# Performance work log

Measured on AMD Instinct MI355X. Metric: run time of the kernel, lower is better.

Reference implementation:

```python
import jax, jax.numpy as jnp
import numpy as np
import math

M = 0.2
S = 30.0
COS_M = math.cos(M); SIN_M = math.sin(M)
TH = math.cos(math.pi - M)          # threshold used in torch.where
MM = math.sin(math.pi - M) * M      # linear penalty past threshold
EPS_LS = 0.1                        # CrossEntropyLoss label_smoothing


def _normalize(a, axis=-1):
    return a / jnp.clip(jnp.linalg.norm(a, axis=axis, keepdims=True), 1e-12)


def setup_inputs() -> dict:
    key = jax.random.key(0)
    k1, k2, k3, k4, k5 = jax.random.split(key, 5)
    B, D, C = 2048, 512, 10000
    x = jax.random.normal(k1, (B, D), dtype=jnp.float32)
    label = jax.random.randint(k2, (B,), 0, 1000)  # valid class ids, ~2 per class
    std = math.sqrt(2.0 / (C + D))  # xavier_normal gain=1
    weight = jax.random.normal(k3, (C, D), dtype=jnp.float32) * std    # self.weight (w)
    weight_m = jax.random.normal(k4, (C, D), dtype=jnp.float32) * std  # self.weight_m (wq)
    weight_n = jax.random.uniform(k5, (C, D), dtype=jnp.float32)       # self.weight_n (wk)
    return {"x": x, "label": label, "weight": weight, "weight_m": weight_m, "weight_n": weight_n}


def reference(x, label, weight, weight_m, weight_n):
    B = x.shape[0]
    C = weight.shape[0]
    xn = _normalize(x)                                   # [B, D]

    # ---- AAM (ArcFace) branch ----
    cosine = xn @ _normalize(weight).T                   # [B, C]
    sine = jnp.sqrt(jnp.clip(1.0 - cosine * cosine, 0.0, 1.0))
    phi = cosine * COS_M - sine * SIN_M
    phi = jnp.where(cosine - TH > 0, phi, cosine - MM)
    one_hot = jax.nn.one_hot(label, C, dtype=cosine.dtype)
    output = (one_hot * phi + (1.0 - one_hot) * cosine) * S
    logp = jax.nn.log_softmax(output, axis=-1)
    q_target = one_hot * (1.0 - EPS_LS) + EPS_LS / C     # label smoothing
    aam_loss = -jnp.mean(jnp.sum(q_target * logp, axis=-1))

    # ---- Control-Contrastive branch ----
    label_matrix = label[:, None] == label[None, :]      # [B, B] bool
    q = xn @ _normalize(weight_m[label]).T               # [B, B]
    k = xn @ _normalize(weight_n[label]).T               # [B, B]
    sim = q * k                                          # elementwise, [B, B]

    lm = label_matrix.astype(sim.dtype)
    ap_m = jnp.sum(sim * lm, axis=1) / jnp.sum(lm, axis=1)  # masked row means, [B]
    ap = jnp.diagonal(sim)                                   # [B]
    an = jnp.where(label_matrix, 0.0, sim)                   # [B, B]

    cos_ap = jnp.clip(ap, 0.0, 1.0)
    sin_ap = jnp.sqrt(jnp.clip(1.0 - cos_ap, 0.0, 1.0))
    cos_apm = jnp.clip(ap_m, 0.0, 1.0)
    sin_apm = jnp.sqrt(jnp.clip(1.0 - cos_apm, 0.0, 1.0))
    cos_an = jnp.clip(an, 0.0, 1.0)
    sin_an = jnp.sqrt(jnp.clip(1.0 - cos_an, 0.0, 1.0))

    phi_pm_c = cos_ap * cos_apm - sin_ap * sin_apm       # [B]
    phi_pm_s = jnp.sqrt(jnp.clip(1.0 - phi_pm_c, 0.0, 1.0))
    phi_pm = phi_pm_c * COS_M - phi_pm_s * SIN_M
    logit_neg = 1.0 - phi_pm                              # [B]

    # torch broadcasting [B,B]*[B] -> broadcast over rows (axis 0)
    phi_nm_s = sin_an * cos_apm[None, :] + cos_an * sin_apm[None, :]
    phi_nm_c = jnp.sqrt(jnp.clip(1.0 - phi_nm_s, 0.0, 1.0))
    phi_nm = phi_nm_s * COS_M - phi_nm_c * SIN_M          # [B, B]

    # ragged boolean-indexed logsumexp == masked logsumexp over whole matrix
    lse_n = jax.nn.logsumexp(jnp.where(label_matrix, -jnp.inf, phi_nm))
    lse_neg = jax.nn.logsumexp(logit_neg)
    cc_loss = jax.nn.softplus(lse_n + lse_neg)

    return aam_loss + cc_loss
```

## Files before the change

kernel.cpp:

```cpp
#include <hip/hip_runtime.h>
#include <hip/hip_bf16.h>

typedef unsigned short u16;
typedef unsigned char u8;
typedef unsigned int u32;
typedef _Float16 f16;
typedef _Float16 f16x8 __attribute__((ext_vector_type(8)));
typedef float f32x4 __attribute__((ext_vector_type(4)));
typedef unsigned int u32x4 __attribute__((ext_vector_type(4)));
typedef unsigned int u32x2 __attribute__((ext_vector_type(2)));
typedef long v2i64 __attribute__((ext_vector_type(2)));

constexpr int BATCH = 2048;
constexpr int DIM   = 512;
constexpr int NCLS  = 10000;
constexpr int NPAD  = 10240;

#define F_S     30.0f
#define F_COS_M 0.9800665778412416f
#define F_SIN_M 0.19866933079506122f
#define F_TH   (-0.9800665778412416f)
#define F_MM    0.03973386615901224f

#define G_AAM  1280
#define G_CC    512

static __device__ __forceinline__ float clampf(float v, float lo, float hi) {
    return fminf(fmaxf(v, lo), hi);
}
static __device__ __forceinline__ u32 pk4_fp8(float a, float b, float c, float d) {
    u32 w = __builtin_amdgcn_cvt_pk_fp8_f32(a, b, 0, false);
    w = __builtin_amdgcn_cvt_pk_fp8_f32(c, d, w, true);
    return w;
}
static __device__ __forceinline__ void glds16(const void* g, void* l) {
    __builtin_amdgcn_global_load_lds(
        (const __attribute__((address_space(1))) unsigned int*)g,
        (__attribute__((address_space(3))) unsigned int*)l, 16, 0, 0);
}
static __device__ __forceinline__ float blk_sum(float v, float* sh, int t) {
#pragma unroll
    for (int o = 32; o > 0; o >>= 1) v += __shfl_down(v, o, 64);
    __syncthreads();
    if ((t & 63) == 0) sh[t >> 6] = v;
    __syncthreads();
    return sh[0] + sh[1] + sh[2] + sh[3];
}

__global__ __launch_bounds__(256) void norm_all_kernel(const float* __restrict__ x,
                                                       const float* __restrict__ w,
                                                       const float* __restrict__ wm,
                                                       const float* __restrict__ wn,
                                                       const int* __restrict__ label,
                                                       u8* __restrict__ xnb,
                                                       u8* __restrict__ wb,
                                                       u8* __restrict__ wqb,
                                                       u8* __restrict__ wkb,
                                                       float* __restrict__ zacc) {
    const int t = threadIdx.x, lane = t & 63, wv = t >> 6;
    const int b = blockIdx.x;
    if (b < 33) zacc[b * 256 + t] = 0.f;

    const int row = b * 4 + wv;
    const float* src;
    u8* dst;
    if (row < BATCH) {
        src = x + (size_t)row * DIM;
        dst = xnb + (size_t)row * DIM;
    } else if (row < BATCH + NPAD) {
        const int r = row - BATCH;
        dst = wb + (size_t)r * DIM;
        if (r >= NCLS) {
            u32x2 z = {0, 0};
            *(u32x2*)(dst + lane * 8) = z;
            return;
        }
        src = w + (size_t)r * DIM;
    } else if (row < BATCH + NPAD + BATCH) {
        const int i = row - (BATCH + NPAD);
        src = wm + (size_t)label[i] * DIM;
        dst = wqb + (size_t)i * DIM;
    } else {
        const int i = row - (BATCH + NPAD + BATCH);
        src = wn + (size_t)label[i] * DIM;
        dst = wkb + (size_t)i * DIM;
    }
    const float4 v0 = ((const float4*)src)[lane * 2];
    const float4 v1 = ((const float4*)src)[lane * 2 + 1];
    float s = v0.x * v0.x + v0.y * v0.y + v0.z * v0.z + v0.w * v0.w
            + v1.x * v1.x + v1.y * v1.y + v1.z * v1.z + v1.w * v1.w;
#pragma unroll
    for (int o = 32; o > 0; o >>= 1) s += __shfl_xor(s, o, 64);
    const float inv = 1.0f / fmaxf(sqrtf(s), 1e-12f);
    u32 lo = pk4_fp8(v0.x * inv, v0.y * inv, v0.z * inv, v0.w * inv);
    u32 hi = pk4_fp8(v1.x * inv, v1.y * inv, v1.z * inv, v1.w * inv);
    const int p = 8 * (lane >> 3) + 4 * (lane & 1) + ((lane >> 1) & 3);
    u32x2 o2;
    o2[0] = __shfl(lo, p, 64);
    o2[1] = __shfl(hi, p, 64);
    *(u32x2*)(dst + lane * 8) = o2;
}

__global__ __launch_bounds__(256) void gemm_fused_kernel(const u8* __restrict__ A,
                                                         const u8* __restrict__ Bw,
                                                         const u8* __restrict__ Bq,
                                                         const u8* __restrict__ Bk,
                                                         const int* __restrict__ label,
                                                         float* __restrict__ sumexp,
                                                         float* __restrict__ sumlogit,
                                                         float* __restrict__ philab,
                                                         f16* __restrict__ sim,
                                                         float* __restrict__ msum,
                                                         float* __restrict__ mcnt,
                                                         float* __restrict__ ap) {
    __shared__ __align__(16) u8 sA[128 * 128];
    __shared__ __align__(16) u8 sB[128 * 128];
    __shared__ float red0[128];
    __shared__ float red1[128];

    const int t = threadIdx.x;
    const int lane = t & 63, wave = t >> 6;
    const int fr = lane & 15, quad = lane >> 4;
    const int swz = fr & 7;

    if (t < 128) { red0[t] = 0.f; red1[t] = 0.f; }

    const int srow = t >> 3;
    const int sgs  = (t & 7) ^ (srow & 7);

    if (blockIdx.x < G_AAM) {
        const int flat = blockIdx.x;
        const int xcd = flat & 7, r = flat >> 3;
        const int bm = r & 15;
        const int bn = (r >> 4) * 8 + xcd;

        const int wm = (wave >> 1) * 64, wn = (wave & 1) * 64;
        const u8* ag = A  + (size_t)(bm * 128 + srow) * DIM + sgs * 16;
        const u8* bg = Bw + (size_t)(bn * 128 + srow) * DIM + sgs * 16;

        f32x4 acc[4][4] = {};

        for (int kb = 0; kb < 4; kb++) {
            const int ko = kb * 128;
#pragma unroll
            for (int s = 0; s < 4; s++) {
                glds16(ag + (size_t)(s * 32) * DIM + ko, &sA[s * 4096 + t * 16]);
                glds16(bg + (size_t)(s * 32) * DIM + ko, &sB[s * 4096 + t * 16]);
            }
            __syncthreads();
#pragma unroll
            for (int blkr = 0; blkr < 2; blkr++) {
                const int slot = ((blkr << 2) | quad) ^ swz;
                v2i64 a8[4], b8[4];
#pragma unroll
                for (int f = 0; f < 4; f++) {
                    a8[f] = __builtin_bit_cast(v2i64, *(const u32x4*)&sA[(wm + f * 16 + fr) * 128 + slot * 16]);
                    b8[f] = __builtin_bit_cast(v2i64, *(const u32x4*)&sB[(wn + f * 16 + fr) * 128 + slot * 16]);
                }
#pragma unroll
                for (int i = 0; i < 4; i++)
#pragma unroll
                    for (int j = 0; j < 4; j++) {
                        acc[i][j] = __builtin_amdgcn_mfma_f32_16x16x32_fp8_fp8(a8[i][0], b8[j][0], acc[i][j], 0, 0, 0);
                        acc[i][j] = __builtin_amdgcn_mfma_f32_16x16x32_fp8_fp8(a8[i][1], b8[j][1], acc[i][j], 0, 0, 0);
                    }
            }
            __syncthreads();
        }

#pragma unroll
        for (int i = 0; i < 4; i++) {
#pragma unroll
            for (int r3 = 0; r3 < 4; r3++) {
                const int ml = wm + i * 16 + quad * 4 + r3;
                const int mg = bm * 128 + ml;
                const int lab = label[mg];
                float esum = 0.f, lsum = 0.f;
#pragma unroll
                for (int j = 0; j < 4; j++) {
                    const int ng = bn * 128 + wn + j * 16 + fr;
                    if (ng < NCLS) {
                        float cv = acc[i][j][r3];
                        float logit;
                        if (ng == lab) {
                            float sine = sqrtf(clampf(1.f - cv * cv, 0.f, 1.f));
                            float phi = cv * F_COS_M - sine * F_SIN_M;
                            float val = ((cv - F_TH) > 0.f) ? phi : (cv - F_MM);
                            logit = F_S * val;
                            philab[mg] = logit;
                        } else {
                            logit = F_S * cv;
                        }
                        esum += __expf(logit);
                        lsum += logit;
                    }
                }
#pragma unroll
                for (int off = 1; off < 16; off <<= 1) {
                    esum += __shfl_xor(esum, off, 64);
                    lsum += __shfl_xor(lsum, off, 64);
                }
                if (fr == 0) {
                    atomicAdd(&red0[ml], esum);
                    atomicAdd(&red1[ml], lsum);
                }
            }
        }
        __syncthreads();
        if (t < 128) {
            atomicAdd(&sumexp[bm * 128 + t], red0[t]);
            atomicAdd(&sumlogit[bm * 128 + t], red1[t]);
        }
    } else {
        const int c = blockIdx.x - G_AAM;
        const int xcd = c & 7, r = c >> 3;
        const int bm = r & 15;
        const int bn = (r >> 4) * 8 + xcd;

        const int wm = (wave >> 1) * 64, wn = (wave & 1) * 32;
        u8* Qs = sB;
        u8* Ks = sB + 8192;

        const u8* ag = A  + (size_t)(bm * 128 + srow) * DIM + sgs * 16;
        const u8* qg = Bq + (size_t)(bn * 64 + srow) * DIM + sgs * 16;
        const u8* kg = Bk + (size_t)(bn * 64 + srow) * DIM + sgs * 16;

        f32x4 aq[4][2] = {};
        f32x4 ak[4][2] = {};

        for (int kb = 0; kb < 4; kb++) {
            const int ko = kb * 128;
#pragma unroll
            for (int s = 0; s < 4; s++)
                glds16(ag + (size_t)(s * 32) * DIM + ko, &sA[s * 4096 + t * 16]);
#pragma unroll
            for (int s = 0; s < 2; s++) {
                glds16(qg + (size_t)(s * 32) * DIM + ko, &Qs[s * 4096 + t * 16]);
                glds16(kg + (size_t)(s * 32) * DIM + ko, &Ks[s * 4096 + t * 16]);
            }
            __syncthreads();
#pragma unroll
            for (int blkr = 0; blkr < 2; blkr++) {
                const int slot = ((blkr << 2) | quad) ^ swz;
                v2i64 a8[4], q8[2], k8[2];
#pragma unroll
                for (int f = 0; f < 4; f++)
                    a8[f] = __builtin_bit_cast(v2i64, *(const u32x4*)&sA[(wm + f * 16 + fr) * 128 + slot * 16]);
#pragma unroll
                for (int f = 0; f < 2; f++) {
                    q8[f] = __builtin_bit_cast(v2i64, *(const u32x4*)&Qs[(wn + f * 16 + fr) * 128 + slot * 16]);
                    k8[f] = __builtin_bit_cast(v2i64, *(const u32x4*)&Ks[(wn + f * 16 + fr) * 128 + slot * 16]);
                }
#pragma unroll
                for (int i = 0; i < 4; i++)
#pragma unroll
                    for (int j = 0; j < 2; j++) {
                        aq[i][j] = __builtin_amdgcn_mfma_f32_16x16x32_fp8_fp8(a8[i][0], q8[j][0], aq[i][j], 0, 0, 0);
                        aq[i][j] = __builtin_amdgcn_mfma_f32_16x16x32_fp8_fp8(a8[i][1], q8[j][1], aq[i][j], 0, 0, 0);
                        ak[i][j] = __builtin_amdgcn_mfma_f32_16x16x32_fp8_fp8(a8[i][0], k8[j][0], ak[i][j], 0, 0, 0);
                        ak[i][j] = __builtin_amdgcn_mfma_f32_16x16x32_fp8_fp8(a8[i][1], k8[j][1], ak[i][j], 0, 0, 0);
                    }
            }
            __syncthreads();
        }

        int lab_n[2];
#pragma unroll
        for (int j = 0; j < 2; j++) lab_n[j] = label[bn * 64 + wn + j * 16 + fr];

#pragma unroll
        for (int i = 0; i < 4; i++) {
#pragma unroll
            for (int r3 = 0; r3 < 4; r3++) {
                const int ml = wm + i * 16 + quad * 4 + r3;
                const int mg = bm * 128 + ml;
                const int lm = label[mg];
                float ms = 0.f, mc = 0.f;
#pragma unroll
                for (int j = 0; j < 2; j++) {
                    const int ng = bn * 64 + wn + j * 16 + fr;
                    float s = aq[i][j][r3] * ak[i][j][r3];
                    sim[(size_t)mg * BATCH + ng] = (f16)s;
                    if (lab_n[j] == lm) { ms += s; mc += 1.f; }
                    if (mg == ng) ap[mg] = s;
                }
#pragma unroll
                for (int off = 1; off < 16; off <<= 1) {
                    ms += __shfl_xor(ms, off, 64);
                    mc += __shfl_xor(mc, off, 64);
                }
                if (fr == 0) {
                    atomicAdd(&red0[ml], ms);
                    atomicAdd(&red1[ml], mc);
                }
            }
        }
        __syncthreads();
        if (t < 128) {
            atomicAdd(&msum[bm * 128 + t], red0[t]);
            atomicAdd(&mcnt[bm * 128 + t], red1[t]);
        }
    }
}

__global__ __launch_bounds__(256) void cc_pass2_kernel(const f16* __restrict__ sim,
                                                       const int* __restrict__ label,
                                                       const float* __restrict__ msum,
                                                       const float* __restrict__ mcnt,
                                                       const float* __restrict__ ap,
                                                       const float* __restrict__ sumexp,
                                                       const float* __restrict__ sumlogit,
                                                       const float* __restrict__ philab,
                                                       float* __restrict__ zn,
                                                       float* __restrict__ zneg,
                                                       float* __restrict__ accA,
                                                       unsigned* __restrict__ tick,
                                                       float* __restrict__ out) {
    __shared__ __align__(16) float cam_s[BATCH];
    __shared__ __align__(16) float sam_s[BATCH];
    __shared__ float sh[4];
    const int t = threadIdx.x, b = blockIdx.x;

    for (int j = t; j < BATCH; j += 256) {
        float cam = clampf(msum[j] / mcnt[j], 0.f, 1.f);
        cam_s[j] = cam;
        sam_s[j] = sqrtf(clampf(1.f - cam, 0.f, 1.f));
    }
    __syncthreads();

    float acc = 0.f;
#pragma unroll
    for (int row = 0; row < 4; row++) {
        const int i = b * 4 + row;
        const int li = label[i];
        const f16x8 v = ((const f16x8*)(sim + (size_t)i * BATCH))[t];
        const int4 l0 = ((const int4*)label)[t * 2];
        const int4 l1 = ((const int4*)label)[t * 2 + 1];
        const f32x4 ca0 = ((const f32x4*)cam_s)[t * 2];
        const f32x4 ca1 = ((const f32x4*)cam_s)[t * 2 + 1];
        const f32x4 sa0 = ((const f32x4*)sam_s)[t * 2];
        const f32x4 sa1 = ((const f32x4*)sam_s)[t * 2 + 1];
#pragma unroll
        for (int e = 0; e < 8; e++) {
            const int lj = (e < 4) ? ((const int*)&l0)[e] : ((const int*)&l1)[e - 4];
            if (lj != li) {
                float can = clampf((float)v[e], 0.f, 1.f);
                float caj = (e < 4) ? ca0[e] : ca1[e - 4];
                float saj = (e < 4) ? sa0[e] : sa1[e - 4];
                float san = sqrtf(clampf(1.f - can, 0.f, 1.f));
                float pns = san * caj + can * saj;
                float pnc = sqrtf(clampf(1.f - pns, 0.f, 1.f));
                acc += __expf(pns * F_COS_M - pnc * F_SIN_M);
            }
        }
    }
    acc = blk_sum(acc, sh, t);

    if (t == 0) {
        float apart = 0.f, epart = 0.f;
#pragma unroll
        for (int row = 0; row < 4; row++) {
            const int rr = b * 4 + row;
            float lse = logf(sumexp[rr]);
            apart += 0.9f * (philab[rr] - lse) + 1e-5f * (sumlogit[rr] - (float)NCLS * lse);
            float cam = cam_s[rr], sam = sam_s[rr];
            float cap = clampf(ap[rr], 0.f, 1.f);
            float sap = sqrtf(clampf(1.f - cap, 0.f, 1.f));
            float ppc = cap * cam - sap * sam;
            float pps = sqrtf(clampf(1.f - ppc, 0.f, 1.f));
            epart += __expf(1.f - (ppc * F_COS_M - pps * F_SIN_M));
        }
        atomicAdd(zn, acc);
        atomicAdd(accA, apart);
        atomicAdd(zneg, epart);
        unsigned old = __hip_atomic_fetch_add(tick, 1u, __ATOMIC_ACQ_REL, __HIP_MEMORY_SCOPE_AGENT);
        if (old == 511u) {
            float znv = __hip_atomic_load(zn,   __ATOMIC_RELAXED, __HIP_MEMORY_SCOPE_AGENT);
            float aav = __hip_atomic_load(accA, __ATOMIC_RELAXED, __HIP_MEMORY_SCOPE_AGENT);
            float zgv = __hip_atomic_load(zneg, __ATOMIC_RELAXED, __HIP_MEMORY_SCOPE_AGENT);
            float aam = -aav / (float)BATCH;
            float z = logf(znv) + logf(zgv);
            float cc = (z > 0.f) ? (z + log1pf(__expf(-z))) : log1pf(__expf(z));
            out[0] = aam + cc;
        }
    }
}

extern "C" void kernel_launch(void* const* d_in, const int* in_sizes, int n_in,
                              void* d_out, int out_size, void* d_ws, size_t ws_size,
                              hipStream_t stream) {
    const float* x        = (const float*)d_in[0];
    const int*   label    = (const int*)d_in[1];
    const float* weight   = (const float*)d_in[2];
    const float* weight_m = (const float*)d_in[3];
    const float* weight_n = (const float*)d_in[4];
    float* out = (float*)d_out;
    char* ws = (char*)d_ws;

    const size_t o_xnb  = 0;
    const size_t o_wb   = o_xnb + (size_t)BATCH * DIM;
    const size_t o_wqb  = o_wb  + (size_t)NPAD * DIM;
    const size_t o_wkb  = o_wqb + (size_t)BATCH * DIM;
    const size_t o_sim  = o_wkb + (size_t)BATCH * DIM;
    const size_t o_misc = o_sim + (size_t)BATCH * BATCH * 2;

    u8* xnb = (u8*)(ws + o_xnb);
    u8* wb  = (u8*)(ws + o_wb);
    u8* wqb = (u8*)(ws + o_wqb);
    u8* wkb = (u8*)(ws + o_wkb);
    f16* sim = (f16*)(ws + o_sim);
    float* mf  = (float*)(ws + o_misc);

    float* sumexp   = mf;
    float* sumlogit = mf + 2048;
    float* msum     = mf + 4096;
    float* mcnt     = mf + 6144;
    float* zn       = mf + 8192;
    float* zneg     = mf + 8193;
    float* accA     = mf + 8194;
    unsigned* tick  = (unsigned*)(mf + 8195);
    float* philab  = mf + 8448;
    float* ap      = mf + 10496;

    norm_all_kernel<<<(BATCH + NPAD + 2 * BATCH) / 4, 256, 0, stream>>>(
        x, weight, weight_m, weight_n, label, xnb, wb, wqb, wkb, mf);

    gemm_fused_kernel<<<G_AAM + G_CC, 256, 0, stream>>>(
        xnb, wb, wqb, wkb, label,
        sumexp, sumlogit, philab, sim, msum, mcnt, ap);

    cc_pass2_kernel<<<512, 256, 0, stream>>>(
        sim, label, msum, mcnt, ap,
        sumexp, sumlogit, philab, zn, zneg, accA, tick, out);
}
```

Before: 183.6 us.

## Load GEMM fragments directly from global memory into registers, dropping LDS staging

Both GEMM branches stop staging A/B tiles in shared memory through global_load_lds with block barriers. Each wave now loads its MFMA fragments straight from global memory into registers, double-buffered across eight K-steps of 64 bytes. This removes LDS traffic and the per-K-block barriers. In exchange, each wave fetches its own copy of operand rows, so operands shared across waves are no longer reused through LDS, and global loads are 16-byte per-lane strided accesses that depend on L2/L1 hits.

```diff
diff --git a/kernel.cpp b/kernel.cpp
--- a/kernel.cpp
+++ b/kernel.cpp
@@ -32,11 +32,6 @@
     u32 w = __builtin_amdgcn_cvt_pk_fp8_f32(a, b, 0, false);
     w = __builtin_amdgcn_cvt_pk_fp8_f32(c, d, w, true);
     return w;
-}
-static __device__ __forceinline__ void glds16(const void* g, void* l) {
-    __builtin_amdgcn_global_load_lds(
-        (const __attribute__((address_space(1))) unsigned int*)g,
-        (__attribute__((address_space(3))) unsigned int*)l, 16, 0, 0);
 }
 static __device__ __forceinline__ float blk_sum(float v, float* sh, int t) {
 #pragma unroll
@@ -113,20 +108,14 @@
                                                          float* __restrict__ msum,
                                                          float* __restrict__ mcnt,
                                                          float* __restrict__ ap) {
-    __shared__ __align__(16) u8 sA[128 * 128];
-    __shared__ __align__(16) u8 sB[128 * 128];
     __shared__ float red0[128];
     __shared__ float red1[128];
 
     const int t = threadIdx.x;
     const int lane = t & 63, wave = t >> 6;
     const int fr = lane & 15, quad = lane >> 4;
-    const int swz = fr & 7;
 
     if (t < 128) { red0[t] = 0.f; red1[t] = 0.f; }
-
-    const int srow = t >> 3;
-    const int sgs  = (t & 7) ^ (srow & 7);
 
     if (blockIdx.x < G_AAM) {
         const int flat = blockIdx.x;
@@ -135,39 +124,42 @@
         const int bn = (r >> 4) * 8 + xcd;
 
         const int wm = (wave >> 1) * 64, wn = (wave & 1) * 64;
-        const u8* ag = A  + (size_t)(bm * 128 + srow) * DIM + sgs * 16;
-        const u8* bg = Bw + (size_t)(bn * 128 + srow) * DIM + sgs * 16;
+        const u8* ar[4];
+        const u8* br[4];
+#pragma unroll
+        for (int f = 0; f < 4; f++) {
+            ar[f] = A  + (size_t)(bm * 128 + wm + f * 16 + fr) * 512 + quad * 16;
+            br[f] = Bw + (size_t)(bn * 128 + wn + f * 16 + fr) * 512 + quad * 16;
+        }
 
         f32x4 acc[4][4] = {};
-
-        for (int kb = 0; kb < 4; kb++) {
-            const int ko = kb * 128;
-#pragma unroll
-            for (int s = 0; s < 4; s++) {
-                glds16(ag + (size_t)(s * 32) * DIM + ko, &sA[s * 4096 + t * 16]);
-                glds16(bg + (size_t)(s * 32) * DIM + ko, &sB[s * 4096 + t * 16]);
+        v2i64 a8[2][4], b8[2][4];
+#pragma unroll
+        for (int f = 0; f < 4; f++) {
+            a8[0][f] = __builtin_bit_cast(v2i64, *(const u32x4*)ar[f]);
+            b8[0][f] = __builtin_bit_cast(v2i64, *(const u32x4*)br[f]);
+        }
+#pragma unroll
+        for (int kb = 0; kb < 8; kb++) {
+            const int cur = kb & 1, nxt = cur ^ 1;
+            if (kb < 7) {
+                const int off = (kb + 1) * 64;
+#pragma unroll
+                for (int f = 0; f < 4; f++) {
+                    a8[nxt][f] = __builtin_bit_cast(v2i64, *(const u32x4*)(ar[f] + off));
+                    b8[nxt][f] = __builtin_bit_cast(v2i64, *(const u32x4*)(br[f] + off));
+                }
             }
-            __syncthreads();
-#pragma unroll
-            for (int blkr = 0; blkr < 2; blkr++) {
-                const int slot = ((blkr << 2) | quad) ^ swz;
-                v2i64 a8[4], b8[4];
-#pragma unroll
-                for (int f = 0; f < 4; f++) {
-                    a8[f] = __builtin_bit_cast(v2i64, *(const u32x4*)&sA[(wm + f * 16 + fr) * 128 + slot * 16]);
-                    b8[f] = __builtin_bit_cast(v2i64, *(const u32x4*)&sB[(wn + f * 16 + fr) * 128 + slot * 16]);
-                }
-#pragma unroll
-                for (int i = 0; i < 4; i++)
-#pragma unroll
-                    for (int j = 0; j < 4; j++) {
-                        acc[i][j] = __builtin_amdgcn_mfma_f32_16x16x32_fp8_fp8(a8[i][0], b8[j][0], acc[i][j], 0, 0, 0);
-                        acc[i][j] = __builtin_amdgcn_mfma_f32_16x16x32_fp8_fp8(a8[i][1], b8[j][1], acc[i][j], 0, 0, 0);
-                    }
-            }
-            __syncthreads();
-        }
-
+#pragma unroll
+            for (int i = 0; i < 4; i++)
+#pragma unroll
+                for (int j = 0; j < 4; j++) {
+                    acc[i][j] = __builtin_amdgcn_mfma_f32_16x16x32_fp8_fp8(a8[cur][i][0], b8[cur][j][0], acc[i][j], 0, 0, 0);
+                    acc[i][j] = __builtin_amdgcn_mfma_f32_16x16x32_fp8_fp8(a8[cur][i][1], b8[cur][j][1], acc[i][j], 0, 0, 0);
+                }
+        }
+
+        __syncthreads();
 #pragma unroll
         for (int i = 0; i < 4; i++) {
 #pragma unroll
@@ -218,56 +210,59 @@
         const int bn = (r >> 4) * 8 + xcd;
 
         const int wm = (wave >> 1) * 64, wn = (wave & 1) * 32;
-        u8* Qs = sB;
-        u8* Ks = sB + 8192;
-
-        const u8* ag = A  + (size_t)(bm * 128 + srow) * DIM + sgs * 16;
-        const u8* qg = Bq + (size_t)(bn * 64 + srow) * DIM + sgs * 16;
-        const u8* kg = Bk + (size_t)(bn * 64 + srow) * DIM + sgs * 16;
+        const u8* ar[4];
+        const u8* qr[2];
+        const u8* kr[2];
+#pragma unroll
+        for (int f = 0; f < 4; f++)
+            ar[f] = A + (size_t)(bm * 128 + wm + f * 16 + fr) * 512 + quad * 16;
+#pragma unroll
+        for (int f = 0; f < 2; f++) {
+            qr[f] = Bq + (size_t)(bn * 64 + wn + f * 16 + fr) * 512 + quad * 16;
+            kr[f] = Bk + (size_t)(bn * 64 + wn + f * 16 + fr) * 512 + quad * 16;
+        }
 
         f32x4 aq[4][2] = {};
         f32x4 ak[4][2] = {};
-
-        for (int kb = 0; kb < 4; kb++) {
-            const int ko = kb * 128;
-#pragma unroll
-            for (int s = 0; s < 4; s++)
-                glds16(ag + (size_t)(s * 32) * DIM + ko, &sA[s * 4096 + t * 16]);
-#pragma unroll
-            for (int s = 0; s < 2; s++) {
-                glds16(qg + (size_t)(s * 32) * DIM + ko, &Qs[s * 4096 + t * 16]);
-                glds16(kg + (size_t)(s * 32) * DIM + ko, &Ks[s * 4096 + t * 16]);
+        v2i64 a8[2][4], q8[2][2], k8[2][2];
+#pragma unroll
+        for (int f = 0; f < 4; f++)
+            a8[0][f] = __builtin_bit_cast(v2i64, *(const u32x4*)ar[f]);
+#pragma unroll
+        for (int f = 0; f < 2; f++) {
+            q8[0][f] = __builtin_bit_cast(v2i64, *(const u32x4*)qr[f]);
+            k8[0][f] = __builtin_bit_cast(v2i64, *(const u32x4*)kr[f]);
+        }
+#pragma unroll
+        for (int kb = 0; kb < 8; kb++) {
+            const int cur = kb & 1, nxt = cur ^ 1;
+            if (kb < 7) {
+                const int off = (kb + 1) * 64;
+#pragma unroll
+                for (int f = 0; f < 4; f++)
+                    a8[nxt][f] = __builtin_bit_cast(v2i64, *(const u32x4*)(ar[f] + off));
+#pragma unroll
+                for (int f = 0; f < 2; f++) {
+                    q8[nxt][f] = __builtin_bit_cast(v2i64, *(const u32x4*)(qr[f] + off));
+                    k8[nxt][f] = __builtin_bit_cast(v2i64, *(const u32x4*)(kr[f] + off));
+                }
             }
-            __syncthreads();
-#pragma unroll
-            for (int blkr = 0; blkr < 2; blkr++) {
-                const int slot = ((blkr << 2) | quad) ^ swz;
-                v2i64 a8[4], q8[2], k8[2];
-#pragma unroll
-                for (int f = 0; f < 4; f++)
-                    a8[f] = __builtin_bit_cast(v2i64, *(const u32x4*)&sA[(wm + f * 16 + fr) * 128 + slot * 16]);
-#pragma unroll
-                for (int f = 0; f < 2; f++) {
-                    q8[f] = __builtin_bit_cast(v2i64, *(const u32x4*)&Qs[(wn + f * 16 + fr) * 128 + slot * 16]);
-                    k8[f] = __builtin_bit_cast(v2i64, *(const u32x4*)&Ks[(wn + f * 16 + fr) * 128 + slot * 16]);
-                }
-#pragma unroll
-                for (int i = 0; i < 4; i++)
-#pragma unroll
-                    for (int j = 0; j < 2; j++) {
-                        aq[i][j] = __builtin_amdgcn_mfma_f32_16x16x32_fp8_fp8(a8[i][0], q8[j][0], aq[i][j], 0, 0, 0);
-                        aq[i][j] = __builtin_amdgcn_mfma_f32_16x16x32_fp8_fp8(a8[i][1], q8[j][1], aq[i][j], 0, 0, 0);
-                        ak[i][j] = __builtin_amdgcn_mfma_f32_16x16x32_fp8_fp8(a8[i][0], k8[j][0], ak[i][j], 0, 0, 0);
-                        ak[i][j] = __builtin_amdgcn_mfma_f32_16x16x32_fp8_fp8(a8[i][1], k8[j][1], ak[i][j], 0, 0, 0);
-                    }
-            }
-            __syncthreads();
+#pragma unroll
+            for (int i = 0; i < 4; i++)
+#pragma unroll
+                for (int j = 0; j < 2; j++) {
+                    aq[i][j] = __builtin_amdgcn_mfma_f32_16x16x32_fp8_fp8(a8[cur][i][0], q8[cur][j][0], aq[i][j], 0, 0, 0);
+                    aq[i][j] = __builtin_amdgcn_mfma_f32_16x16x32_fp8_fp8(a8[cur][i][1], q8[cur][j][1], aq[i][j], 0, 0, 0);
+                    ak[i][j] = __builtin_amdgcn_mfma_f32_16x16x32_fp8_fp8(a8[cur][i][0], k8[cur][j][0], ak[i][j], 0, 0, 0);
+                    ak[i][j] = __builtin_amdgcn_mfma_f32_16x16x32_fp8_fp8(a8[cur][i][1], k8[cur][j][1], ak[i][j], 0, 0, 0);
+                }
         }
 
         int lab_n[2];
 #pragma unroll
         for (int j = 0; j < 2; j++) lab_n[j] = label[bn * 64 + wn + j * 16 + fr];
 
+        __syncthreads();
 #pragma unroll
         for (int i = 0; i < 4; i++) {
 #pragma unroll
```

New measurement: 223.1 us. 21.5% more time.

## Double-buffer LDS tiles with 64-wide K steps to overlap loads and MFMA

Applied to the files above, without the earlier changes.

Replaces the single 128-wide K tile, which was loaded and then consumed between two barriers, with two 64-wide LDS buffers. The next K slice is prefetched into one buffer while MFMAs run on the other, leaving one barrier per step. The swizzle is changed to a 4-slot XOR pattern to match the narrower rows. The total LDS footprint stays the same, but there are twice as many loop iterations and barriers, and the new swizzle may cause different bank conflicts.

```diff
diff --git a/kernel.cpp b/kernel.cpp
--- a/kernel.cpp
+++ b/kernel.cpp
@@ -113,20 +113,20 @@
                                                          float* __restrict__ msum,
                                                          float* __restrict__ mcnt,
                                                          float* __restrict__ ap) {
-    __shared__ __align__(16) u8 sA[128 * 128];
-    __shared__ __align__(16) u8 sB[128 * 128];
+    __shared__ __align__(16) u8 sA[2][8192];
+    __shared__ __align__(16) u8 sB[2][8192];
     __shared__ float red0[128];
     __shared__ float red1[128];
 
     const int t = threadIdx.x;
     const int lane = t & 63, wave = t >> 6;
     const int fr = lane & 15, quad = lane >> 4;
-    const int swz = fr & 7;
+    const int slot = quad ^ (fr & 3);
 
     if (t < 128) { red0[t] = 0.f; red1[t] = 0.f; }
 
-    const int srow = t >> 3;
-    const int sgs  = (t & 7) ^ (srow & 7);
+    const int srow = t >> 2;
+    const int sgr  = (t & 3) ^ (srow & 3);
 
     if (blockIdx.x < G_AAM) {
         const int flat = blockIdx.x;
@@ -135,37 +135,41 @@
         const int bn = (r >> 4) * 8 + xcd;
 
         const int wm = (wave >> 1) * 64, wn = (wave & 1) * 64;
-        const u8* ag = A  + (size_t)(bm * 128 + srow) * DIM + sgs * 16;
-        const u8* bg = Bw + (size_t)(bn * 128 + srow) * DIM + sgs * 16;
+        const u8* ag0 = A  + (size_t)(bm * 128 + srow) * 512 + sgr * 16;
+        const u8* ag1 = ag0 + (size_t)64 * 512;
+        const u8* bg0 = Bw + (size_t)(bn * 128 + srow) * 512 + sgr * 16;
+        const u8* bg1 = bg0 + (size_t)64 * 512;
+
+        glds16(ag0, &sA[0][t * 16]);
+        glds16(ag1, &sA[0][4096 + t * 16]);
+        glds16(bg0, &sB[0][t * 16]);
+        glds16(bg1, &sB[0][4096 + t * 16]);
 
         f32x4 acc[4][4] = {};
-
-        for (int kb = 0; kb < 4; kb++) {
-            const int ko = kb * 128;
-#pragma unroll
-            for (int s = 0; s < 4; s++) {
-                glds16(ag + (size_t)(s * 32) * DIM + ko, &sA[s * 4096 + t * 16]);
-                glds16(bg + (size_t)(s * 32) * DIM + ko, &sB[s * 4096 + t * 16]);
-            }
+#pragma unroll
+        for (int kb = 0; kb < 8; kb++) {
+            const int cur = kb & 1;
             __syncthreads();
-#pragma unroll
-            for (int blkr = 0; blkr < 2; blkr++) {
-                const int slot = ((blkr << 2) | quad) ^ swz;
-                v2i64 a8[4], b8[4];
-#pragma unroll
-                for (int f = 0; f < 4; f++) {
-                    a8[f] = __builtin_bit_cast(v2i64, *(const u32x4*)&sA[(wm + f * 16 + fr) * 128 + slot * 16]);
-                    b8[f] = __builtin_bit_cast(v2i64, *(const u32x4*)&sB[(wn + f * 16 + fr) * 128 + slot * 16]);
-                }
-#pragma unroll
-                for (int i = 0; i < 4; i++)
-#pragma unroll
-                    for (int j = 0; j < 4; j++) {
-                        acc[i][j] = __builtin_amdgcn_mfma_f32_16x16x32_fp8_fp8(a8[i][0], b8[j][0], acc[i][j], 0, 0, 0);
-                        acc[i][j] = __builtin_amdgcn_mfma_f32_16x16x32_fp8_fp8(a8[i][1], b8[j][1], acc[i][j], 0, 0, 0);
-                    }
-            }
-            __syncthreads();
+            if (kb < 7) {
+                const int ko = (kb + 1) * 64;
+                glds16(ag0 + ko, &sA[cur ^ 1][t * 16]);
+                glds16(ag1 + ko, &sA[cur ^ 1][4096 + t * 16]);
+                glds16(bg0 + ko, &sB[cur ^ 1][t * 16]);
+                glds16(bg1 + ko, &sB[cur ^ 1][4096 + t * 16]);
+            }
+            v2i64 a8[4], b8[4];
+#pragma unroll
+            for (int f = 0; f < 4; f++) {
+                a8[f] = __builtin_bit_cast(v2i64, *(const u32x4*)&sA[cur][(wm + f * 16 + fr) * 64 + slot * 16]);
+                b8[f] = __builtin_bit_cast(v2i64, *(const u32x4*)&sB[cur][(wn + f * 16 + fr) * 64 + slot * 16]);
+            }
+#pragma unroll
+            for (int i = 0; i < 4; i++)
+#pragma unroll
+                for (int j = 0; j < 4; j++) {
+                    acc[i][j] = __builtin_amdgcn_mfma_f32_16x16x32_fp8_fp8(a8[i][0], b8[j][0], acc[i][j], 0, 0, 0);
+                    acc[i][j] = __builtin_amdgcn_mfma_f32_16x16x32_fp8_fp8(a8[i][1], b8[j][1], acc[i][j], 0, 0, 0);
+                }
         }
 
 #pragma unroll
@@ -218,50 +222,47 @@
         const int bn = (r >> 4) * 8 + xcd;
 
         const int wm = (wave >> 1) * 64, wn = (wave & 1) * 32;
-        u8* Qs = sB;
-        u8* Ks = sB + 8192;
-
-        const u8* ag = A  + (size_t)(bm * 128 + srow) * DIM + sgs * 16;
-        const u8* qg = Bq + (size_t)(bn * 64 + srow) * DIM + sgs * 16;
-        const u8* kg = Bk + (size_t)(bn * 64 + srow) * DIM + sgs * 16;
+        const u8* ag0 = A  + (size_t)(bm * 128 + srow) * 512 + sgr * 16;
+        const u8* ag1 = ag0 + (size_t)64 * 512;
+        const u8* qg  = Bq + (size_t)(bn * 64 + srow) * 512 + sgr * 16;
+        const u8* kg  = Bk + (size_t)(bn * 64 + srow) * 512 + sgr * 16;
+
+        glds16(ag0, &sA[0][t * 16]);
+        glds16(ag1, &sA[0][4096 + t * 16]);
+        glds16(qg,  &sB[0][t * 16]);
+        glds16(kg,  &sB[0][4096 + t * 16]);
 
         f32x4 aq[4][2] = {};
         f32x4 ak[4][2] = {};
-
-        for (int kb = 0; kb < 4; kb++) {
-            const int ko = kb * 128;
-#pragma unroll
-            for (int s = 0; s < 4; s++)
-                glds16(ag + (size_t)(s * 32) * DIM + ko, &sA[s * 4096 + t * 16]);
-#pragma unroll
-            for (int s = 0; s < 2; s++) {
-                glds16(qg + (size_t)(s * 32) * DIM + ko, &Qs[s * 4096 + t * 16]);
-                glds16(kg + (size_t)(s * 32) * DIM + ko, &Ks[s * 4096 + t * 16]);
-            }
+#pragma unroll
+        for (int kb = 0; kb < 8; kb++) {
+            const int cur = kb & 1;
             __syncthreads();
-#pragma unroll
-            for (int blkr = 0; blkr < 2; blkr++) {
-                const int slot = ((blkr << 2) | quad) ^ swz;
-                v2i64 a8[4], q8[2], k8[2];
-#pragma unroll
-                for (int f = 0; f < 4; f++)
-                    a8[f] = __builtin_bit_cast(v2i64, *(const u32x4*)&sA[(wm + f * 16 + fr) * 128 + slot * 16]);
-#pragma unroll
-                for (int f = 0; f < 2; f++) {
-                    q8[f] = __builtin_bit_cast(v2i64, *(const u32x4*)&Qs[(wn + f * 16 + fr) * 128 + slot * 16]);
-                    k8[f] = __builtin_bit_cast(v2i64, *(const u32x4*)&Ks[(wn + f * 16 + fr) * 128 + slot * 16]);
-                }
-#pragma unroll
-                for (int i = 0; i < 4; i++)
-#pragma unroll
-                    for (int j = 0; j < 2; j++) {
-                        aq[i][j] = __builtin_amdgcn_mfma_f32_16x16x32_fp8_fp8(a8[i][0], q8[j][0], aq[i][j], 0, 0, 0);
-                        aq[i][j] = __builtin_amdgcn_mfma_f32_16x16x32_fp8_fp8(a8[i][1], q8[j][1], aq[i][j], 0, 0, 0);
-                        ak[i][j] = __builtin_amdgcn_mfma_f32_16x16x32_fp8_fp8(a8[i][0], k8[j][0], ak[i][j], 0, 0, 0);
-                        ak[i][j] = __builtin_amdgcn_mfma_f32_16x16x32_fp8_fp8(a8[i][1], k8[j][1], ak[i][j], 0, 0, 0);
-                    }
-            }
-            __syncthreads();
+            if (kb < 7) {
+                const int ko = (kb + 1) * 64;
+                glds16(ag0 + ko, &sA[cur ^ 1][t * 16]);
+                glds16(ag1 + ko, &sA[cur ^ 1][4096 + t * 16]);
+                glds16(qg + ko,  &sB[cur ^ 1][t * 16]);
+                glds16(kg + ko,  &sB[cur ^ 1][4096 + t * 16]);
+            }
+            v2i64 a8[4], q8[2], k8[2];
+#pragma unroll
+            for (int f = 0; f < 4; f++)
+                a8[f] = __builtin_bit_cast(v2i64, *(const u32x4*)&sA[cur][(wm + f * 16 + fr) * 64 + slot * 16]);
+#pragma unroll
+            for (int f = 0; f < 2; f++) {
+                q8[f] = __builtin_bit_cast(v2i64, *(const u32x4*)&sB[cur][(wn + f * 16 + fr) * 64 + slot * 16]);
+                k8[f] = __builtin_bit_cast(v2i64, *(const u32x4*)&sB[cur][4096 + (wn + f * 16 + fr) * 64 + slot * 16]);
+            }
+#pragma unroll
+            for (int i = 0; i < 4; i++)
+#pragma unroll
+                for (int j = 0; j < 2; j++) {
+                    aq[i][j] = __builtin_amdgcn_mfma_f32_16x16x32_fp8_fp8(a8[i][0], q8[j][0], aq[i][j], 0, 0, 0);
+                    aq[i][j] = __builtin_amdgcn_mfma_f32_16x16x32_fp8_fp8(a8[i][1], q8[j][1], aq[i][j], 0, 0, 0);
+                    ak[i][j] = __builtin_amdgcn_mfma_f32_16x16x32_fp8_fp8(a8[i][0], k8[j][0], ak[i][j], 0, 0, 0);
+                    ak[i][j] = __builtin_amdgcn_mfma_f32_16x16x32_fp8_fp8(a8[i][1], k8[j][1], ak[i][j], 0, 0, 0);
+                }
         }
 
         int lab_n[2];
```

Result: slower. 188.6 us (+2.7%).
